# Kernel tuning notes

Measured on AMD Instinct MI355X. Metric: run time of the kernel, lower is better.

## Reference

```python
import jax, jax.numpy as jnp
import numpy as np

N_NODES = 50000
N_EDGES = 800000
D_FEAT = 64


def setup_inputs() -> dict:
    key = jax.random.key(0)
    k1, k2, k3 = jax.random.split(key, 3)
    x_sum = jax.random.normal(k1, (N_NODES, D_FEAT), dtype=jnp.float32)
    x_prod = jax.random.uniform(k2, (N_NODES, D_FEAT), dtype=jnp.float32)
    edge_index = jax.random.randint(k3, (2, N_EDGES), 0, N_NODES, dtype=jnp.int64)
    return {"x_sum": x_sum, "x_prod": x_prod, "edge_index": edge_index}


def reference(x_sum, x_prod, edge_index):
    # flow='source_to_target' -> gather from edge_index[0], aggregate at edge_index[1]
    src_idx = edge_index[0]
    dst_idx = edge_index[1]
    n = x_sum.shape[0]

    # __lift__: index_select along node dim (message is identity; edge_attr/norm None)
    m_sum = x_sum[src_idx]    # [E, D]
    m_prod = x_prod[src_idx]  # [E, D]

    # scatter_sum: zeros-init + scatter_add_
    out_sum = jax.ops.segment_sum(m_sum, dst_idx, num_segments=n)

    # scatter_product: ones-init + scatter_(reduce='multiply')
    out_prod = jnp.ones((n, x_prod.shape[1]), dtype=x_prod.dtype).at[dst_idx].multiply(m_prod)

    return out_sum, out_prod
```

## Files before the change

### kernel.cpp

```cpp
#include <hip/hip_runtime.h>
#include <hip/hip_fp16.h>

#define N_NODES 50000
#define N_EDGES 800000
#define D_FEAT  64
#define BSHIFT  6
#define NBKT    782
#define NB      256
#define CHUNK   3125
#define CAST_CHUNK 12500
#define PSHIFT  20
#define SRC_MASK ((1 << PSHIFT) - 1)

#define WS_FLAG    0
#define WS_TOT     64
#define WS_COFF    (WS_TOT + NBKT)
#define WS_BH      (WS_COFF + NBKT + 1)
#define WS_OFFS    (WS_BH + NBKT * NB)
#define WS_PAIR    (WS_OFFS + N_NODES + 1)
#define WS_SSRC    (WS_PAIR + N_EDGES)
#define WS_PACKED  (WS_SSRC + N_EDGES)
#define WS_INTS    (WS_PACKED + N_NODES * D_FEAT)

__device__ inline int detect_idx_layout_local(const int* idx) {
    int allzero = 1;
    #pragma unroll
    for (int i = 1; i < 129; i += 2) {
        if (idx[i] != 0) allzero = 0;
    }
    return allzero;
}

__global__ __launch_bounds__(256) void cast_hist(int* __restrict__ W,
                                                 const int* __restrict__ idx,
                                                 const float* __restrict__ xs,
                                                 const float* __restrict__ xp) {
    __shared__ int h[NBKT];
    for (int i = threadIdx.x; i < NBKT; i += 256) h[i] = 0;
    __syncthreads();

    const int flg = detect_idx_layout_local(idx);
    const int t = threadIdx.x;

    __half2* packed = (__half2*)(W + WS_PACKED);
    const int cbase = blockIdx.x * CAST_CHUNK;
    for (int i = cbase + t; i < cbase + CAST_CHUNK; i += 256)
        packed[i] = __floats2half2_rn(xs[i], xp[i]);

    const int base = blockIdx.x * CHUNK;
    for (int e = base + t; e < base + CHUNK; e += 256) {
        int dst = flg ? idx[2 * (N_EDGES + e)] : idx[N_EDGES + e];
        atomicAdd(&h[dst >> BSHIFT], 1);
    }
    __syncthreads();
    for (int i = t; i < NBKT; i += 256)
        W[WS_BH + i * NB + blockIdx.x] = h[i];
    if (blockIdx.x == 0 && t == 0) {
        W[WS_FLAG] = flg;
        W[WS_OFFS + N_NODES] = N_EDGES;
    }
}

__global__ __launch_bounds__(256) void bucket_scan(int* __restrict__ W) {
    __shared__ int part[NB];
    int j = blockIdx.x;
    int t = threadIdx.x;
    int c = W[WS_BH + j * NB + t];
    part[t] = c;
    __syncthreads();
    for (int off = 1; off < NB; off <<= 1) {
        int u = (t >= off) ? part[t - off] : 0;
        __syncthreads();
        part[t] += u;
        __syncthreads();
    }
    W[WS_BH + j * NB + t] = part[t] - c;
    if (t == NB - 1) W[WS_TOT + j] = part[t];
}

__global__ __launch_bounds__(1024) void base_scan(int* __restrict__ W) {
    __shared__ int part[1024];
    int t = threadIdx.x;
    int v = (t < NBKT) ? W[WS_TOT + t] : 0;
    part[t] = v;
    __syncthreads();
    for (int off = 1; off < 1024; off <<= 1) {
        int u = (t >= off) ? part[t - off] : 0;
        __syncthreads();
        part[t] += u;
        __syncthreads();
    }
    if (t < NBKT) W[WS_COFF + t] = part[t] - v;
    if (t == 0) W[WS_COFF + NBKT] = N_EDGES;
}

__global__ __launch_bounds__(256) void coarse_scatter(const int* __restrict__ idx,
                                                      int* __restrict__ W) {
    __shared__ int cur[NBKT];
    for (int i = threadIdx.x; i < NBKT; i += 256)
        cur[i] = W[WS_COFF + i] + W[WS_BH + i * NB + blockIdx.x];
    __syncthreads();
    const int flg = W[WS_FLAG];
    const int base = blockIdx.x * CHUNK;
    for (int e = base + threadIdx.x; e < base + CHUNK; e += 256) {
        int src, dst;
        if (flg) { src = idx[2 * e]; dst = idx[2 * (N_EDGES + e)]; }
        else     { src = idx[e];     dst = idx[N_EDGES + e]; }
        int pos = atomicAdd(&cur[dst >> BSHIFT], 1);
        W[WS_PAIR + pos] = src | ((dst & 63) << PSHIFT);
    }
}

__global__ __launch_bounds__(256) void fine_sort(int* __restrict__ W) {
    __shared__ int h[4][64];
    int b = blockIdx.x;
    int t = threadIdx.x;
    int w = t >> 6;
    int lane = t & 63;
    int bbase = W[WS_COFF + b];
    int bend  = W[WS_COFF + b + 1];
    h[w][lane] = 0;
    __syncthreads();
    for (int e = bbase + t; e < bend; e += 256)
        atomicAdd(&h[w][(unsigned)W[WS_PAIR + e] >> PSHIFT], 1);
    __syncthreads();
    if (t < 64) {
        int c0 = h[0][t], c1 = h[1][t], c2 = h[2][t], c3 = h[3][t];
        int tot = c0 + c1 + c2 + c3;
        int incl = tot;
        #pragma unroll
        for (int off = 1; off < 64; off <<= 1) {
            int u = __shfl_up(incl, off, 64);
            if (t >= off) incl += u;
        }
        int excl = incl - tot;
        int node = (b << BSHIFT) + t;
        if (node < N_NODES) W[WS_OFFS + node] = bbase + excl;
        h[0][t] = excl;
        h[1][t] = excl + c0;
        h[2][t] = excl + c0 + c1;
        h[3][t] = excl + c0 + c1 + c2;
    }
    __syncthreads();
    for (int e = bbase + t; e < bend; e += 256) {
        int v = W[WS_PAIR + e];
        int p = atomicAdd(&h[w][(unsigned)v >> PSHIFT], 1);
        W[WS_SSRC + bbase + p] = v & SRC_MASK;
    }
}

__global__ __launch_bounds__(256) void gather_reduce(const int* __restrict__ W,
                                                     float* __restrict__ out) {
    int wave = (int)((blockIdx.x * blockDim.x + threadIdx.x) >> 6);
    int lane = threadIdx.x & 63;
    if (wave >= N_NODES) return;
    int beg = __builtin_amdgcn_readfirstlane(W[WS_OFFS + wave]);
    int end = __builtin_amdgcn_readfirstlane(W[WS_OFFS + wave + 1]);
    const int* ssrc = W + WS_SSRC;
    const __half2* packed = (const __half2*)(W + WS_PACKED);

    float s0 = 0.f, s1 = 0.f, s2 = 0.f, s3 = 0.f;
    float s4 = 0.f, s5 = 0.f, s6 = 0.f, s7 = 0.f;
    float p0 = 1.f, p1 = 1.f, p2 = 1.f, p3 = 1.f;
    float p4 = 1.f, p5 = 1.f, p6 = 1.f, p7 = 1.f;
    int i = beg;
    for (; i + 15 < end; i += 16) {
        float2 f[16];
        #pragma unroll
        for (int k = 0; k < 16; ++k)
            f[k] = __half22float2(packed[ssrc[i + k] * D_FEAT + lane]);
        s0 += f[0].x + f[8].x;  s1 += f[1].x + f[9].x;
        s2 += f[2].x + f[10].x; s3 += f[3].x + f[11].x;
        s4 += f[4].x + f[12].x; s5 += f[5].x + f[13].x;
        s6 += f[6].x + f[14].x; s7 += f[7].x + f[15].x;
        p0 *= f[0].y * f[8].y;  p1 *= f[1].y * f[9].y;
        p2 *= f[2].y * f[10].y; p3 *= f[3].y * f[11].y;
        p4 *= f[4].y * f[12].y; p5 *= f[5].y * f[13].y;
        p6 *= f[6].y * f[14].y; p7 *= f[7].y * f[15].y;
    }
    for (; i + 3 < end; i += 4) {
        float2 f0 = __half22float2(packed[ssrc[i] * D_FEAT + lane]);
        float2 f1 = __half22float2(packed[ssrc[i + 1] * D_FEAT + lane]);
        float2 f2 = __half22float2(packed[ssrc[i + 2] * D_FEAT + lane]);
        float2 f3 = __half22float2(packed[ssrc[i + 3] * D_FEAT + lane]);
        s0 += f0.x; s1 += f1.x; s2 += f2.x; s3 += f3.x;
        p0 *= f0.y; p1 *= f1.y; p2 *= f2.y; p3 *= f3.y;
    }
    for (; i < end; ++i) {
        float2 f = __half22float2(packed[ssrc[i] * D_FEAT + lane]);
        s0 += f.x;
        p0 *= f.y;
    }
    float ssum = ((s0 + s1) + (s2 + s3)) + ((s4 + s5) + (s6 + s7));
    float pprd = ((p0 * p1) * (p2 * p3)) * ((p4 * p5) * (p6 * p7));
    out[(long)wave * D_FEAT + lane] = ssum;
    out[(long)N_NODES * D_FEAT + (long)wave * D_FEAT + lane] = pprd;
}

__device__ inline void atomicMulF32(float* addr, float val) {
    unsigned int* ua = (unsigned int*)addr;
    unsigned int old = __hip_atomic_load(ua, __ATOMIC_RELAXED, __HIP_MEMORY_SCOPE_AGENT);
    while (true) {
        unsigned int assumed = old;
        unsigned int desired = __float_as_uint(__uint_as_float(assumed) * val);
        old = atomicCAS(ua, assumed, desired);
        if (old == assumed) break;
    }
}

__global__ void fb_init(float* __restrict__ out, int* __restrict__ flag,
                        const int* __restrict__ idx) {
    const int n4 = (N_NODES * D_FEAT) / 4;
    int tid = blockIdx.x * blockDim.x + threadIdx.x;
    int stride = gridDim.x * blockDim.x;
    float4* o = (float4*)out;
    const float4 z = make_float4(0.f, 0.f, 0.f, 0.f);
    const float4 one = make_float4(1.f, 1.f, 1.f, 1.f);
    for (int i = tid; i < n4; i += stride) { o[i] = z; o[n4 + i] = one; }
    if (blockIdx.x == 0 && threadIdx.x == 0) *flag = detect_idx_layout_local(idx);
}

__global__ void fb_scatter(const float* __restrict__ xs, const float* __restrict__ xp,
                           const int* __restrict__ idx, float* __restrict__ out,
                           const int* __restrict__ flag) {
    long tid = (long)blockIdx.x * blockDim.x + threadIdx.x;
    const long total = (long)N_EDGES * (D_FEAT / 4);
    if (tid >= total) return;
    int e = (int)(tid >> 4);
    int c = (int)(tid & 15);
    int src, dst;
    if (*flag) { src = idx[2 * e]; dst = idx[2 * (N_EDGES + e)]; }
    else       { src = idx[e];     dst = idx[N_EDGES + e]; }
    const float4 s = ((const float4*)(xs + (long)src * D_FEAT))[c];
    const float4 p = ((const float4*)(xp + (long)src * D_FEAT))[c];
    float* os = out + (long)dst * D_FEAT + c * 4;
    float* op = out + (long)N_NODES * D_FEAT + (long)dst * D_FEAT + c * 4;
    atomicAdd(os + 0, s.x); atomicAdd(os + 1, s.y);
    atomicAdd(os + 2, s.z); atomicAdd(os + 3, s.w);
    atomicMulF32(op + 0, p.x); atomicMulF32(op + 1, p.y);
    atomicMulF32(op + 2, p.z); atomicMulF32(op + 3, p.w);
}

extern "C" void kernel_launch(void* const* d_in, const int* in_sizes, int n_in,
                              void* d_out, int out_size, void* d_ws, size_t ws_size,
                              hipStream_t stream) {
    const float* x_sum  = (const float*)d_in[0];
    const float* x_prod = (const float*)d_in[1];
    const int*   eidx   = (const int*)d_in[2];
    float* out = (float*)d_out;
    int* W = (int*)d_ws;

    if (ws_size < (size_t)WS_INTS * sizeof(int)) {
        fb_init<<<1024, 256, 0, stream>>>(out, W, eidx);
        const long total = (long)N_EDGES * (D_FEAT / 4);
        int grid = (int)((total + 255) / 256);
        fb_scatter<<<grid, 256, 0, stream>>>(x_sum, x_prod, eidx, out, W);
        return;
    }

    cast_hist<<<NB, 256, 0, stream>>>(W, eidx, x_sum, x_prod);
    bucket_scan<<<NBKT, 256, 0, stream>>>(W);
    base_scan<<<1, 1024, 0, stream>>>(W);
    coarse_scatter<<<NB, 256, 0, stream>>>(eidx, W);
    fine_sort<<<NBKT, 256, 0, stream>>>(W);
    gather_reduce<<<(N_NODES + 3) / 4, 256, 0, stream>>>(W, out);
}
```

Baseline: 154.1 us.

## Fold base scan into bucket scan via last-block pattern; rebalance unrolls

Removes the separate single-block base_scan launch by having the last bucket_scan block to finish (detected through an atomic counter with thread fences) compute the exclusive scan of bucket totals, four per thread. coarse_scatter is unrolled to issue four index loads before the shared atomics, and gather_reduce drops its 16-wide unroll for an 8-wide loop with the source indices loaded first. These target launch overhead and load latency. In exchange they add a serialized tail to the last block and change register pressure in the gather.

```diff
diff --git a/kernel.cpp b/kernel.cpp
--- a/kernel.cpp
+++ b/kernel.cpp
@@ -13,6 +13,7 @@
 #define SRC_MASK ((1 << PSHIFT) - 1)
 
 #define WS_FLAG    0
+#define WS_DONE    1
 #define WS_TOT     64
 #define WS_COFF    (WS_TOT + NBKT)
 #define WS_BH      (WS_COFF + NBKT + 1)
@@ -57,12 +58,14 @@
         W[WS_BH + i * NB + blockIdx.x] = h[i];
     if (blockIdx.x == 0 && t == 0) {
         W[WS_FLAG] = flg;
+        W[WS_DONE] = 0;
         W[WS_OFFS + N_NODES] = N_EDGES;
     }
 }
 
 __global__ __launch_bounds__(256) void bucket_scan(int* __restrict__ W) {
     __shared__ int part[NB];
+    __shared__ int islast;
     int j = blockIdx.x;
     int t = threadIdx.x;
     int c = W[WS_BH + j * NB + t];
@@ -76,21 +79,38 @@
     }
     W[WS_BH + j * NB + t] = part[t] - c;
     if (t == NB - 1) W[WS_TOT + j] = part[t];
-}
-
-__global__ __launch_bounds__(1024) void base_scan(int* __restrict__ W) {
-    __shared__ int part[1024];
-    int t = threadIdx.x;
-    int v = (t < NBKT) ? W[WS_TOT + t] : 0;
-    part[t] = v;
-    __syncthreads();
-    for (int off = 1; off < 1024; off <<= 1) {
+    __syncthreads();
+
+    if (t == 0) {
+        __threadfence();
+        int old = atomicAdd(&W[WS_DONE], 1);
+        islast = (old == NBKT - 1);
+    }
+    __syncthreads();
+    if (!islast) return;
+
+    __threadfence();
+    int base4 = t * 4;
+    int c4[4];
+    #pragma unroll
+    for (int k = 0; k < 4; ++k)
+        c4[k] = (base4 + k < NBKT) ? W[WS_TOT + base4 + k] : 0;
+    int local = c4[0] + c4[1] + c4[2] + c4[3];
+    __syncthreads();
+    part[t] = local;
+    __syncthreads();
+    for (int off = 1; off < NB; off <<= 1) {
         int u = (t >= off) ? part[t - off] : 0;
         __syncthreads();
         part[t] += u;
         __syncthreads();
     }
-    if (t < NBKT) W[WS_COFF + t] = part[t] - v;
+    int run = part[t] - local;
+    #pragma unroll
+    for (int k = 0; k < 4; ++k) {
+        if (base4 + k < NBKT) W[WS_COFF + base4 + k] = run;
+        run += c4[k];
+    }
     if (t == 0) W[WS_COFF + NBKT] = N_EDGES;
 }
 
@@ -101,8 +121,25 @@
         cur[i] = W[WS_COFF + i] + W[WS_BH + i * NB + blockIdx.x];
     __syncthreads();
     const int flg = W[WS_FLAG];
+    const int t = threadIdx.x;
     const int base = blockIdx.x * CHUNK;
-    for (int e = base + threadIdx.x; e < base + CHUNK; e += 256) {
+    const int lim = base + CHUNK;
+    int e = base + t;
+    for (; e + 768 < lim; e += 1024) {
+        int s4[4], d4[4];
+        #pragma unroll
+        for (int k = 0; k < 4; ++k) {
+            int ee = e + k * 256;
+            if (flg) { s4[k] = idx[2 * ee]; d4[k] = idx[2 * (N_EDGES + ee)]; }
+            else     { s4[k] = idx[ee];     d4[k] = idx[N_EDGES + ee]; }
+        }
+        #pragma unroll
+        for (int k = 0; k < 4; ++k) {
+            int pos = atomicAdd(&cur[d4[k] >> BSHIFT], 1);
+            W[WS_PAIR + pos] = s4[k] | ((d4[k] & 63) << PSHIFT);
+        }
+    }
+    for (; e < lim; e += 256) {
         int src, dst;
         if (flg) { src = idx[2 * e]; dst = idx[2 * (N_EDGES + e)]; }
         else     { src = idx[e];     dst = idx[N_EDGES + e]; }
@@ -164,29 +201,30 @@
     float p0 = 1.f, p1 = 1.f, p2 = 1.f, p3 = 1.f;
     float p4 = 1.f, p5 = 1.f, p6 = 1.f, p7 = 1.f;
     int i = beg;
-    for (; i + 15 < end; i += 16) {
-        float2 f[16];
-        #pragma unroll
-        for (int k = 0; k < 16; ++k)
-            f[k] = __half22float2(packed[ssrc[i + k] * D_FEAT + lane]);
-        s0 += f[0].x + f[8].x;  s1 += f[1].x + f[9].x;
-        s2 += f[2].x + f[10].x; s3 += f[3].x + f[11].x;
-        s4 += f[4].x + f[12].x; s5 += f[5].x + f[13].x;
-        s6 += f[6].x + f[14].x; s7 += f[7].x + f[15].x;
-        p0 *= f[0].y * f[8].y;  p1 *= f[1].y * f[9].y;
-        p2 *= f[2].y * f[10].y; p3 *= f[3].y * f[11].y;
-        p4 *= f[4].y * f[12].y; p5 *= f[5].y * f[13].y;
-        p6 *= f[6].y * f[14].y; p7 *= f[7].y * f[15].y;
-    }
-    for (; i + 3 < end; i += 4) {
-        float2 f0 = __half22float2(packed[ssrc[i] * D_FEAT + lane]);
-        float2 f1 = __half22float2(packed[ssrc[i + 1] * D_FEAT + lane]);
-        float2 f2 = __half22float2(packed[ssrc[i + 2] * D_FEAT + lane]);
-        float2 f3 = __half22float2(packed[ssrc[i + 3] * D_FEAT + lane]);
+    for (; i + 7 < end; i += 8) {
+        int a0 = ssrc[i],     a1 = ssrc[i + 1], a2 = ssrc[i + 2], a3 = ssrc[i + 3];
+        int a4 = ssrc[i + 4], a5 = ssrc[i + 5], a6 = ssrc[i + 6], a7 = ssrc[i + 7];
+        float2 f0 = __half22float2(packed[a0 * D_FEAT + lane]);
+        float2 f1 = __half22float2(packed[a1 * D_FEAT + lane]);
+        float2 f2 = __half22float2(packed[a2 * D_FEAT + lane]);
+        float2 f3 = __half22float2(packed[a3 * D_FEAT + lane]);
+        float2 f4 = __half22float2(packed[a4 * D_FEAT + lane]);
+        float2 f5 = __half22float2(packed[a5 * D_FEAT + lane]);
+        float2 f6 = __half22float2(packed[a6 * D_FEAT + lane]);
+        float2 f7 = __half22float2(packed[a7 * D_FEAT + lane]);
         s0 += f0.x; s1 += f1.x; s2 += f2.x; s3 += f3.x;
+        s4 += f4.x; s5 += f5.x; s6 += f6.x; s7 += f7.x;
         p0 *= f0.y; p1 *= f1.y; p2 *= f2.y; p3 *= f3.y;
-    }
-    for (; i < end; ++i) {
+        p4 *= f4.y; p5 *= f5.y; p6 *= f6.y; p7 *= f7.y;
+    }
+    for (; i + 1 < end; i += 2) {
+        int a0 = ssrc[i], a1 = ssrc[i + 1];
+        float2 f0 = __half22float2(packed[a0 * D_FEAT + lane]);
+        float2 f1 = __half22float2(packed[a1 * D_FEAT + lane]);
+        s0 += f0.x; s1 += f1.x;
+        p0 *= f0.y; p1 *= f1.y;
+    }
+    if (i < end) {
         float2 f = __half22float2(packed[ssrc[i] * D_FEAT + lane]);
         s0 += f.x;
         p0 *= f.y;
@@ -260,7 +298,6 @@
 
     cast_hist<<<NB, 256, 0, stream>>>(W, eidx, x_sum, x_prod);
     bucket_scan<<<NBKT, 256, 0, stream>>>(W);
-    base_scan<<<1, 1024, 0, stream>>>(W);
     coarse_scatter<<<NB, 256, 0, stream>>>(eidx, W);
     fine_sort<<<NBKT, 256, 0, stream>>>(W);
     gather_reduce<<<(N_NODES + 3) / 4, 256, 0, stream>>>(W, out);
```

After: 180.6 us. 17.2% more time.

## Fuse fine sort with gather-reduce in LDS and fold base scan into scatter

Applied to the files above, without the earlier changes.

Drops the single-block base_scan launch by having every coarse_scatter block redo the small bucket-total scan with wave shuffles; block 0 writes the offsets for later use. Fine_sort and gather_reduce become one sort_gather kernel: each 512-thread block sorts its bucket's sources into shared memory and then reduces its 64 nodes directly, skipping the global sorted-source array and two launches. Buckets larger than MAXB fall back to a global buffer. The cost is fewer, larger blocks for the gather phase (782 blocks of 8 waves, each wave handling 8 nodes in sequence) and a shorter unroll, which may reduce memory-level parallelism.

```diff
diff --git a/kernel.cpp b/kernel.cpp
--- a/kernel.cpp
+++ b/kernel.cpp
@@ -11,6 +11,7 @@
 #define CAST_CHUNK 12500
 #define PSHIFT  20
 #define SRC_MASK ((1 << PSHIFT) - 1)
+#define MAXB    2048
 
 #define WS_FLAG    0
 #define WS_TOT     64
@@ -55,10 +56,7 @@
     __syncthreads();
     for (int i = t; i < NBKT; i += 256)
         W[WS_BH + i * NB + blockIdx.x] = h[i];
-    if (blockIdx.x == 0 && t == 0) {
-        W[WS_FLAG] = flg;
-        W[WS_OFFS + N_NODES] = N_EDGES;
-    }
+    if (blockIdx.x == 0 && t == 0) W[WS_FLAG] = flg;
 }
 
 __global__ __launch_bounds__(256) void bucket_scan(int* __restrict__ W) {
@@ -78,31 +76,51 @@
     if (t == NB - 1) W[WS_TOT + j] = part[t];
 }
 
-__global__ __launch_bounds__(1024) void base_scan(int* __restrict__ W) {
-    __shared__ int part[1024];
-    int t = threadIdx.x;
-    int v = (t < NBKT) ? W[WS_TOT + t] : 0;
-    part[t] = v;
-    __syncthreads();
-    for (int off = 1; off < 1024; off <<= 1) {
-        int u = (t >= off) ? part[t - off] : 0;
-        __syncthreads();
-        part[t] += u;
-        __syncthreads();
-    }
-    if (t < NBKT) W[WS_COFF + t] = part[t] - v;
-    if (t == 0) W[WS_COFF + NBKT] = N_EDGES;
-}
-
 __global__ __launch_bounds__(256) void coarse_scatter(const int* __restrict__ idx,
                                                       int* __restrict__ W) {
+    __shared__ int coff[NBKT + 1];
     __shared__ int cur[NBKT];
-    for (int i = threadIdx.x; i < NBKT; i += 256)
-        cur[i] = W[WS_COFF + i] + W[WS_BH + i * NB + blockIdx.x];
-    __syncthreads();
+    __shared__ int wsum[4];
+    const int t = threadIdx.x;
+    const int w = t >> 6;
+    const int lane = t & 63;
+
+    int base4 = t * 4;
+    int c4[4];
+    #pragma unroll
+    for (int k = 0; k < 4; ++k)
+        c4[k] = (base4 + k < NBKT) ? W[WS_TOT + base4 + k] : 0;
+    int local = c4[0] + c4[1] + c4[2] + c4[3];
+    int incl = local;
+    #pragma unroll
+    for (int off = 1; off < 64; off <<= 1) {
+        int u = __shfl_up(incl, off, 64);
+        if (lane >= off) incl += u;
+    }
+    if (lane == 63) wsum[w] = incl;
+    __syncthreads();
+    int woff = 0;
+    #pragma unroll
+    for (int k = 0; k < 4; ++k) if (k < w) woff += wsum[k];
+    int run = incl + woff - local;
+    #pragma unroll
+    for (int k = 0; k < 4; ++k) {
+        if (base4 + k < NBKT) coff[base4 + k] = run;
+        run += c4[k];
+    }
+    if (t == 0) coff[NBKT] = N_EDGES;
+    __syncthreads();
+
+    if (blockIdx.x == 0)
+        for (int i = t; i <= NBKT; i += 256) W[WS_COFF + i] = coff[i];
+
+    for (int i = t; i < NBKT; i += 256)
+        cur[i] = coff[i] + W[WS_BH + i * NB + blockIdx.x];
+    __syncthreads();
+
     const int flg = W[WS_FLAG];
     const int base = blockIdx.x * CHUNK;
-    for (int e = base + threadIdx.x; e < base + CHUNK; e += 256) {
+    for (int e = base + t; e < base + CHUNK; e += 256) {
         int src, dst;
         if (flg) { src = idx[2 * e]; dst = idx[2 * (N_EDGES + e)]; }
         else     { src = idx[e];     dst = idx[N_EDGES + e]; }
@@ -111,22 +129,71 @@
     }
 }
 
-__global__ __launch_bounds__(256) void fine_sort(int* __restrict__ W) {
-    __shared__ int h[4][64];
-    int b = blockIdx.x;
-    int t = threadIdx.x;
-    int w = t >> 6;
-    int lane = t & 63;
-    int bbase = W[WS_COFF + b];
-    int bend  = W[WS_COFF + b + 1];
+#define GATHER_BODY(SRCS)                                                          \
+    {                                                                              \
+        float s0 = 0.f, s1 = 0.f, s2 = 0.f, s3 = 0.f;                              \
+        float s4 = 0.f, s5 = 0.f, s6 = 0.f, s7 = 0.f;                              \
+        float p0 = 1.f, p1 = 1.f, p2 = 1.f, p3 = 1.f;                              \
+        float p4 = 1.f, p5 = 1.f, p6 = 1.f, p7 = 1.f;                              \
+        int i = beg;                                                               \
+        for (; i + 7 < end; i += 8) {                                              \
+            int a0 = SRCS[i],     a1 = SRCS[i + 1], a2 = SRCS[i + 2], a3 = SRCS[i + 3]; \
+            int a4 = SRCS[i + 4], a5 = SRCS[i + 5], a6 = SRCS[i + 6], a7 = SRCS[i + 7]; \
+            float2 f0 = __half22float2(packed[a0 * D_FEAT + lane]);                \
+            float2 f1 = __half22float2(packed[a1 * D_FEAT + lane]);                \
+            float2 f2 = __half22float2(packed[a2 * D_FEAT + lane]);                \
+            float2 f3 = __half22float2(packed[a3 * D_FEAT + lane]);                \
+            float2 f4 = __half22float2(packed[a4 * D_FEAT + lane]);                \
+            float2 f5 = __half22float2(packed[a5 * D_FEAT + lane]);                \
+            float2 f6 = __half22float2(packed[a6 * D_FEAT + lane]);                \
+            float2 f7 = __half22float2(packed[a7 * D_FEAT + lane]);                \
+            s0 += f0.x; s1 += f1.x; s2 += f2.x; s3 += f3.x;                        \
+            s4 += f4.x; s5 += f5.x; s6 += f6.x; s7 += f7.x;                        \
+            p0 *= f0.y; p1 *= f1.y; p2 *= f2.y; p3 *= f3.y;                        \
+            p4 *= f4.y; p5 *= f5.y; p6 *= f6.y; p7 *= f7.y;                        \
+        }                                                                          \
+        for (; i + 1 < end; i += 2) {                                              \
+            int a0 = SRCS[i], a1 = SRCS[i + 1];                                    \
+            float2 f0 = __half22float2(packed[a0 * D_FEAT + lane]);                \
+            float2 f1 = __half22float2(packed[a1 * D_FEAT + lane]);                \
+            s0 += f0.x; s1 += f1.x;                                                \
+            p0 *= f0.y; p1 *= f1.y;                                                \
+        }                                                                          \
+        if (i < end) {                                                             \
+            float2 f = __half22float2(packed[SRCS[i] * D_FEAT + lane]);            \
+            s0 += f.x;                                                             \
+            p0 *= f.y;                                                             \
+        }                                                                          \
+        float ssum = ((s0 + s1) + (s2 + s3)) + ((s4 + s5) + (s6 + s7));            \
+        float pprd = ((p0 * p1) * (p2 * p3)) * ((p4 * p5) * (p6 * p7));            \
+        out[(long)node * D_FEAT + lane] = ssum;                                    \
+        out[(long)N_NODES * D_FEAT + (long)node * D_FEAT + lane] = pprd;           \
+    }
+
+__global__ __launch_bounds__(512) void sort_gather(int* __restrict__ W,
+                                                   float* __restrict__ out) {
+    __shared__ int h[8][64];
+    __shared__ int offs[65];
+    __shared__ int lssrc[MAXB];
+    const int j = blockIdx.x;
+    const int t = threadIdx.x;
+    const int w = t >> 6;
+    const int lane = t & 63;
+    const int bbase = W[WS_COFF + j];
+    const int bend  = W[WS_COFF + j + 1];
+    const int cnt   = bend - bbase;
+    const __half2* packed = (const __half2*)(W + WS_PACKED);
+
     h[w][lane] = 0;
     __syncthreads();
-    for (int e = bbase + t; e < bend; e += 256)
+    for (int e = bbase + t; e < bend; e += 512)
         atomicAdd(&h[w][(unsigned)W[WS_PAIR + e] >> PSHIFT], 1);
     __syncthreads();
     if (t < 64) {
-        int c0 = h[0][t], c1 = h[1][t], c2 = h[2][t], c3 = h[3][t];
-        int tot = c0 + c1 + c2 + c3;
+        int cc[8];
+        int tot = 0;
+        #pragma unroll
+        for (int k = 0; k < 8; ++k) { cc[k] = h[k][t]; tot += cc[k]; }
         int incl = tot;
         #pragma unroll
         for (int off = 1; off < 64; off <<= 1) {
@@ -134,67 +201,44 @@
             if (t >= off) incl += u;
         }
         int excl = incl - tot;
-        int node = (b << BSHIFT) + t;
-        if (node < N_NODES) W[WS_OFFS + node] = bbase + excl;
-        h[0][t] = excl;
-        h[1][t] = excl + c0;
-        h[2][t] = excl + c0 + c1;
-        h[3][t] = excl + c0 + c1 + c2;
-    }
-    __syncthreads();
-    for (int e = bbase + t; e < bend; e += 256) {
-        int v = W[WS_PAIR + e];
-        int p = atomicAdd(&h[w][(unsigned)v >> PSHIFT], 1);
-        W[WS_SSRC + bbase + p] = v & SRC_MASK;
-    }
-}
-
-__global__ __launch_bounds__(256) void gather_reduce(const int* __restrict__ W,
-                                                     float* __restrict__ out) {
-    int wave = (int)((blockIdx.x * blockDim.x + threadIdx.x) >> 6);
-    int lane = threadIdx.x & 63;
-    if (wave >= N_NODES) return;
-    int beg = __builtin_amdgcn_readfirstlane(W[WS_OFFS + wave]);
-    int end = __builtin_amdgcn_readfirstlane(W[WS_OFFS + wave + 1]);
-    const int* ssrc = W + WS_SSRC;
-    const __half2* packed = (const __half2*)(W + WS_PACKED);
-
-    float s0 = 0.f, s1 = 0.f, s2 = 0.f, s3 = 0.f;
-    float s4 = 0.f, s5 = 0.f, s6 = 0.f, s7 = 0.f;
-    float p0 = 1.f, p1 = 1.f, p2 = 1.f, p3 = 1.f;
-    float p4 = 1.f, p5 = 1.f, p6 = 1.f, p7 = 1.f;
-    int i = beg;
-    for (; i + 15 < end; i += 16) {
-        float2 f[16];
+        offs[t] = excl;
+        if (t == 63) offs[64] = incl;
+        int r = excl;
         #pragma unroll
-        for (int k = 0; k < 16; ++k)
-            f[k] = __half22float2(packed[ssrc[i + k] * D_FEAT + lane]);
-        s0 += f[0].x + f[8].x;  s1 += f[1].x + f[9].x;
-        s2 += f[2].x + f[10].x; s3 += f[3].x + f[11].x;
-        s4 += f[4].x + f[12].x; s5 += f[5].x + f[13].x;
-        s6 += f[6].x + f[14].x; s7 += f[7].x + f[15].x;
-        p0 *= f[0].y * f[8].y;  p1 *= f[1].y * f[9].y;
-        p2 *= f[2].y * f[10].y; p3 *= f[3].y * f[11].y;
-        p4 *= f[4].y * f[12].y; p5 *= f[5].y * f[13].y;
-        p6 *= f[6].y * f[14].y; p7 *= f[7].y * f[15].y;
-    }
-    for (; i + 3 < end; i += 4) {
-        float2 f0 = __half22float2(packed[ssrc[i] * D_FEAT + lane]);
-        float2 f1 = __half22float2(packed[ssrc[i + 1] * D_FEAT + lane]);
-        float2 f2 = __half22float2(packed[ssrc[i + 2] * D_FEAT + lane]);
-        float2 f3 = __half22float2(packed[ssrc[i + 3] * D_FEAT + lane]);
-        s0 += f0.x; s1 += f1.x; s2 += f2.x; s3 += f3.x;
-        p0 *= f0.y; p1 *= f1.y; p2 *= f2.y; p3 *= f3.y;
-    }
-    for (; i < end; ++i) {
-        float2 f = __half22float2(packed[ssrc[i] * D_FEAT + lane]);
-        s0 += f.x;
-        p0 *= f.y;
-    }
-    float ssum = ((s0 + s1) + (s2 + s3)) + ((s4 + s5) + (s6 + s7));
-    float pprd = ((p0 * p1) * (p2 * p3)) * ((p4 * p5) * (p6 * p7));
-    out[(long)wave * D_FEAT + lane] = ssum;
-    out[(long)N_NODES * D_FEAT + (long)wave * D_FEAT + lane] = pprd;
+        for (int k = 0; k < 8; ++k) { h[k][t] = r; r += cc[k]; }
+    }
+    __syncthreads();
+
+    if (cnt <= MAXB) {
+        for (int e = bbase + t; e < bend; e += 512) {
+            int v = W[WS_PAIR + e];
+            int p = atomicAdd(&h[w][(unsigned)v >> PSHIFT], 1);
+            lssrc[p] = v & SRC_MASK;
+        }
+        __syncthreads();
+        for (int nl = w * 8; nl < w * 8 + 8; ++nl) {
+            int node = (j << BSHIFT) + nl;
+            if (node >= N_NODES) break;
+            int beg = __builtin_amdgcn_readfirstlane(offs[nl]);
+            int end = __builtin_amdgcn_readfirstlane(offs[nl + 1]);
+            GATHER_BODY(lssrc)
+        }
+    } else {
+        int* gs = W + WS_SSRC + bbase;
+        for (int e = bbase + t; e < bend; e += 512) {
+            int v = W[WS_PAIR + e];
+            int p = atomicAdd(&h[w][(unsigned)v >> PSHIFT], 1);
+            gs[p] = v & SRC_MASK;
+        }
+        __syncthreads();
+        for (int nl = w * 8; nl < w * 8 + 8; ++nl) {
+            int node = (j << BSHIFT) + nl;
+            if (node >= N_NODES) break;
+            int beg = __builtin_amdgcn_readfirstlane(offs[nl]);
+            int end = __builtin_amdgcn_readfirstlane(offs[nl + 1]);
+            GATHER_BODY(gs)
+        }
+    }
 }
 
 __device__ inline void atomicMulF32(float* addr, float val) {
@@ -260,8 +304,6 @@
 
     cast_hist<<<NB, 256, 0, stream>>>(W, eidx, x_sum, x_prod);
     bucket_scan<<<NBKT, 256, 0, stream>>>(W);
-    base_scan<<<1, 1024, 0, stream>>>(W);
     coarse_scatter<<<NB, 256, 0, stream>>>(eidx, W);
-    fine_sort<<<NBKT, 256, 0, stream>>>(W);
-    gather_reduce<<<(N_NODES + 3) / 4, 256, 0, stream>>>(W, out);
-}
+    sort_gather<<<NBKT, 512, 0, stream>>>(W, out);
+}
```

Result: slower. 160.0 us (+3.8%).
